# Kernel optimization log

Measured on AMD Instinct MI355X. Metric: run time of the kernel, lower is better.

Reference implementation:

```python
import jax, jax.numpy as jnp
import numpy as np

B, C, T = 8, 256, 4096
IC = C // 2  # inter_channels
BN_EPS = 1e-5


def setup_inputs() -> dict:
    key = jax.random.key(0)
    ks = jax.random.split(key, 12)
    s_in = 1.0 / np.sqrt(C)
    s_ic = 1.0 / np.sqrt(IC)
    return {
        "x": jax.random.normal(ks[0], (B, C, T), dtype=jnp.float32),
        "theta_w": jax.random.uniform(ks[1], (IC, C), jnp.float32, -s_in, s_in),
        "theta_b": jax.random.uniform(ks[2], (IC,), jnp.float32, -s_in, s_in),
        "phi_w": jax.random.uniform(ks[3], (IC, C), jnp.float32, -s_in, s_in),
        "phi_b": jax.random.uniform(ks[4], (IC,), jnp.float32, -s_in, s_in),
        "g_w": jax.random.uniform(ks[5], (IC, C), jnp.float32, -s_in, s_in),
        "g_b": jax.random.uniform(ks[6], (IC,), jnp.float32, -s_in, s_in),
        "w_w": jax.random.uniform(ks[7], (C, IC), jnp.float32, -s_ic, s_ic),
        "w_b": jax.random.uniform(ks[8], (C,), jnp.float32, -s_ic, s_ic),
        "bn_gamma": jax.random.normal(ks[9], (C,), dtype=jnp.float32),
        "bn_beta": jax.random.normal(ks[10], (C,), dtype=jnp.float32),
    }


def _conv1x1(w, b, inp):
    # Conv1d kernel_size=1 == per-position channel matmul
    return jnp.einsum('oc,bct->bot', w, inp) + b[None, :, None]


def _maxpool2(z):
    b, c, t = z.shape
    return z.reshape(b, c, t // 2, 2).max(axis=-1)


def reference(x, theta_w, theta_b, phi_w, phi_b, g_w, g_b, w_w, w_b, bn_gamma, bn_beta):
    theta_x = _conv1x1(theta_w, theta_b, x)              # (B, IC, T)
    phi_x = _maxpool2(_conv1x1(phi_w, phi_b, x))         # (B, IC, T/2)
    g_x = _maxpool2(_conv1x1(g_w, g_b, x))               # (B, IC, T/2)

    # f = theta^T @ phi ; softmax-free, divided by N = T/2
    f = jnp.einsum('bct,bcs->bts', theta_x, phi_x)       # (B, T, T/2)
    f_div_C = f / f.shape[-1]
    y = jnp.einsum('bts,bcs->bct', f_div_C, g_x)         # (B, IC, T)

    w_y = _conv1x1(w_w, w_b, y)                          # (B, C, T)
    # BatchNorm1d (training-mode batch statistics over batch+time)
    mean = w_y.mean(axis=(0, 2), keepdims=True)
    var = w_y.var(axis=(0, 2), keepdims=True)
    w_y = (w_y - mean) * jax.lax.rsqrt(var + BN_EPS)
    w_y = w_y * bn_gamma[None, :, None] + bn_beta[None, :, None]
    return w_y + x
```

## Files before the change

kernel.cpp:

```cpp
#include <hip/hip_runtime.h>
#include <hip/hip_bf16.h>

typedef __attribute__((ext_vector_type(8))) short short8;
typedef __attribute__((ext_vector_type(4))) short short4v;
typedef __attribute__((ext_vector_type(4))) float floatx4;
typedef unsigned int u32;

#define BB 8
#define CC 256
#define ICH 128
#define TT 4096
#define SS 2048
static constexpr float BN_EPS = 1e-5f;
static constexpr float INV_S  = 1.0f / 2048.0f;
static constexpr float INV_BT = 1.0f / 32768.0f;

typedef const __attribute__((address_space(1))) u32* gas_ptr;
typedef __attribute__((address_space(3))) u32* las_ptr;
__device__ __forceinline__ void gl_lds16(const void* g, void* l) {
    __builtin_amdgcn_global_load_lds((gas_ptr)g, (las_ptr)l, 16, 0, 0);
}

__global__ __launch_bounds__(256) void k0x_transpose(
    const float* __restrict__ x, __hip_bfloat16* __restrict__ xt)
{
    __shared__ float Tl[64][65];
    const int b = blockIdx.z, cb = blockIdx.y * 64, tb = blockIdx.x * 64;
    const int tid = threadIdx.x;
    #pragma unroll
    for (int it = 0; it < 4; ++it) {
        int idx = tid + 256 * it;
        int row = idx >> 4, c4 = idx & 15;
        float4 v = *(const float4*)(x + ((size_t)b * CC + cb + row) * TT + tb + c4 * 4);
        Tl[row][c4 * 4 + 0] = v.x; Tl[row][c4 * 4 + 1] = v.y;
        Tl[row][c4 * 4 + 2] = v.z; Tl[row][c4 * 4 + 3] = v.w;
    }
    __syncthreads();
    #pragma unroll
    for (int it = 0; it < 2; ++it) {
        int idx = tid + 256 * it;
        int trow = idx >> 3, ch = idx & 7;
        alignas(16) __hip_bfloat16 tmp[8];
        #pragma unroll
        for (int e = 0; e < 8; ++e) tmp[e] = __float2bfloat16(Tl[ch * 8 + e][trow]);
        *(short8*)(xt + ((size_t)b * TT + tb + trow) * CC + cb + ch * 8) = *(const short8*)tmp;
    }
}

__global__ __launch_bounds__(256) void k0w_conv(
    const float* __restrict__ phi_w, const float* __restrict__ g_w,
    __hip_bfloat16* __restrict__ Wf)
{
    int idx = blockIdx.x * 256 + threadIdx.x;
    const float* src = (idx < 8192) ? (phi_w + (size_t)idx * 4)
                                    : (g_w + (size_t)(idx - 8192) * 4);
    float4 v = *(const float4*)src;
    alignas(8) __hip_bfloat16 t[4];
    t[0] = __float2bfloat16(v.x); t[1] = __float2bfloat16(v.y);
    t[2] = __float2bfloat16(v.z); t[3] = __float2bfloat16(v.w);
    *(short4v*)(Wf + (size_t)idx * 4) = *(const short4v*)t;
}

__global__ __launch_bounds__(256) void k1_mfma(
    const __hip_bfloat16* __restrict__ Wf, const float* __restrict__ phi_b,
    const float* __restrict__ g_b, const __hip_bfloat16* __restrict__ xt,
    __hip_bfloat16* __restrict__ phi_g)
{
    __shared__ short lds[128 * 132];
    short* As = lds;
    short* Bs = lds + 128 * 64;

    const int b  = blockIdx.z;
    const int m0 = blockIdx.y * 128;
    const int tb = blockIdx.x * 128;
    const int s0 = blockIdx.x * 64;
    const int tid = threadIdx.x;
    const int w = tid >> 6, l = tid & 63;
    const int quad = l >> 4, lm = l & 15;
    const int wm = (w & 1) * 64, wn = (w >> 1) * 64;
    const int rs = l >> 3, cs = (l & 7) * 8;

    const __hip_bfloat16* Ap = Wf + (size_t)m0 * CC;
    const __hip_bfloat16* Bp = xt + ((size_t)b * TT + tb) * CC;

    floatx4 acc[4][4];
    #pragma unroll
    for (int i = 0; i < 4; ++i)
        #pragma unroll
        for (int j = 0; j < 4; ++j) acc[i][j] = (floatx4)0.f;

    for (int kc = 0; kc < 4; ++kc) {
        const int k0 = kc * 64;
        const int rbase = w * 32;
        #pragma unroll
        for (int t = 0; t < 4; ++t) {
            gl_lds16(Ap + (size_t)(rbase + t * 8 + rs) * CC + k0 + cs, &As[(rbase + t * 8) * 64]);
            gl_lds16(Bp + (size_t)(rbase + t * 8 + rs) * CC + k0 + cs, &Bs[(rbase + t * 8) * 64]);
        }
        __syncthreads();
        #pragma unroll
        for (int ks = 0; ks < 2; ++ks) {
            short8 a[4], bb[4];
            #pragma unroll
            for (int i = 0; i < 4; ++i)
                a[i] = *(const short8*)&As[(wm + i * 16 + lm) * 64 + ks * 32 + quad * 8];
            #pragma unroll
            for (int j = 0; j < 4; ++j)
                bb[j] = *(const short8*)&Bs[(wn + j * 16 + lm) * 64 + ks * 32 + quad * 8];
            #pragma unroll
            for (int i = 0; i < 4; ++i)
                #pragma unroll
                for (int j = 0; j < 4; ++j)
                    acc[i][j] = __builtin_amdgcn_mfma_f32_16x16x32_bf16(a[i], bb[j], acc[i][j], 0, 0, 0);
        }
        __syncthreads();
    }

    __hip_bfloat16* Out = (__hip_bfloat16*)lds;
    #pragma unroll
    for (int i = 0; i < 4; ++i)
        #pragma unroll
        for (int j = 0; j < 4; ++j)
            #pragma unroll
            for (int r = 0; r < 4; ++r)
                Out[(wm + i * 16 + quad * 4 + r) * 132 + wn + j * 16 + lm] =
                    __float2bfloat16(acc[i][j][r]);
    __syncthreads();
    #pragma unroll
    for (int it = 0; it < 4; ++it) {
        int idx = tid + 256 * it;
        int orow = idx >> 3, grp = idx & 7;
        int o = m0 + orow;
        float bias = (o < ICH) ? phi_b[o] : g_b[o - ICH];
        short8 v0 = *(const short8*)&Out[orow * 132 + grp * 16];
        short8 v1 = *(const short8*)&Out[orow * 132 + grp * 16 + 8];
        const __hip_bfloat16* p0 = (const __hip_bfloat16*)&v0;
        const __hip_bfloat16* p1 = (const __hip_bfloat16*)&v1;
        alignas(16) __hip_bfloat16 o8[8];
        #pragma unroll
        for (int e = 0; e < 4; ++e)
            o8[e] = __float2bfloat16(
                fmaxf(__bfloat162float(p0[2 * e]), __bfloat162float(p0[2 * e + 1])) + bias);
        #pragma unroll
        for (int e = 0; e < 4; ++e)
            o8[4 + e] = __float2bfloat16(
                fmaxf(__bfloat162float(p1[2 * e]), __bfloat162float(p1[2 * e + 1])) + bias);
        *(short8*)(phi_g + ((size_t)b * CC + o) * SS + s0 + grp * 8) = *(const short8*)o8;
    }
}

__global__ __launch_bounds__(256) void k2_mfma(
    const __hip_bfloat16* __restrict__ phi_g, float* __restrict__ Mpart)
{
    __shared__ short lds[2 * 128 * 64];
    short* As = lds;
    short* Bs = lds + 128 * 64;
    const int sc = blockIdx.x, b = blockIdx.y;
    const int tid = threadIdx.x;
    const int w = tid >> 6, l = tid & 63;
    const int quad = l >> 4, lm = l & 15;
    const int wm = (w & 1) * 64, wn = (w >> 1) * 64;
    const int rs = l >> 3, cs = (l & 7) * 8;

    const __hip_bfloat16* Ap = phi_g + (size_t)b * CC * SS + sc * 128;
    const __hip_bfloat16* Bp = Ap + (size_t)ICH * SS;

    floatx4 acc[4][4];
    #pragma unroll
    for (int i = 0; i < 4; ++i)
        #pragma unroll
        for (int j = 0; j < 4; ++j) acc[i][j] = (floatx4)0.f;

    for (int kc = 0; kc < 2; ++kc) {
        const int k0 = kc * 64;
        const int rbase = w * 32;
        #pragma unroll
        for (int t = 0; t < 4; ++t) {
            gl_lds16(Ap + (size_t)(rbase + t * 8 + rs) * SS + k0 + cs, &As[(rbase + t * 8) * 64]);
            gl_lds16(Bp + (size_t)(rbase + t * 8 + rs) * SS + k0 + cs, &Bs[(rbase + t * 8) * 64]);
        }
        __syncthreads();
        #pragma unroll
        for (int ks = 0; ks < 2; ++ks) {
            short8 a[4], bb[4];
            #pragma unroll
            for (int i = 0; i < 4; ++i)
                a[i] = *(const short8*)&As[(wm + i * 16 + lm) * 64 + ks * 32 + quad * 8];
            #pragma unroll
            for (int j = 0; j < 4; ++j)
                bb[j] = *(const short8*)&Bs[(wn + j * 16 + lm) * 64 + ks * 32 + quad * 8];
            #pragma unroll
            for (int i = 0; i < 4; ++i)
                #pragma unroll
                for (int j = 0; j < 4; ++j)
                    acc[i][j] = __builtin_amdgcn_mfma_f32_16x16x32_bf16(a[i], bb[j], acc[i][j], 0, 0, 0);
        }
        __syncthreads();
    }

    float* dst = Mpart + ((size_t)(b * 16 + sc)) * ICH * ICH;
    #pragma unroll
    for (int i = 0; i < 4; ++i)
        #pragma unroll
        for (int j = 0; j < 4; ++j)
            #pragma unroll
            for (int r = 0; r < 4; ++r)
                dst[(size_t)(wm + i * 16 + quad * 4 + r) * ICH + wn + j * 16 + lm] = acc[i][j][r];
}

__global__ __launch_bounds__(256) void k2b_reduce(
    const float* __restrict__ Mpart, float* __restrict__ Msum)
{
    const int b = blockIdx.y;
    const size_t f4 = (size_t)blockIdx.x * 256 + threadIdx.x;
    const float* src = Mpart + (size_t)b * 16 * 16384 + f4 * 4;
    float4 s = {0.f, 0.f, 0.f, 0.f};
    #pragma unroll
    for (int sc = 0; sc < 16; ++sc) {
        float4 v = *(const float4*)(src + (size_t)sc * 16384);
        s.x += v.x; s.y += v.y; s.z += v.z; s.w += v.w;
    }
    *(float4*)(Msum + (size_t)b * 16384 + f4 * 4) = s;
}

__global__ __launch_bounds__(256) void k3a_kb(
    const float* __restrict__ w_w, const float* __restrict__ Msum,
    float* __restrict__ Kb)
{
    __shared__ float Al[64][65];
    __shared__ float Bl[64][65];
    const int b = blockIdx.z;
    const int cob = blockIdx.y * 64;
    const int cpb = blockIdx.x * 64;
    const int tid = threadIdx.x;
    const int tx = tid & 15, ty = tid >> 4;

    float acc[4][4] = {};
    for (int kc2 = 0; kc2 < 2; ++kc2) {
        #pragma unroll
        for (int r = 0; r < 4; ++r) {
            int idx = tid + 256 * r;
            int row = idx >> 4, c4 = idx & 15;
            float4 v = *(const float4*)(w_w + (size_t)(cob + row) * ICH + kc2 * 64 + c4 * 4);
            Al[c4 * 4 + 0][row] = v.x; Al[c4 * 4 + 1][row] = v.y;
            Al[c4 * 4 + 2][row] = v.z; Al[c4 * 4 + 3][row] = v.w;
            float4 m = *(const float4*)(Msum + ((size_t)b * ICH + cpb + row) * ICH + kc2 * 64 + c4 * 4);
            Bl[c4 * 4 + 0][row] = m.x; Bl[c4 * 4 + 1][row] = m.y;
            Bl[c4 * 4 + 2][row] = m.z; Bl[c4 * 4 + 3][row] = m.w;
        }
        __syncthreads();
        for (int k = 0; k < 64; ++k) {
            float av[4], bv[4];
            #pragma unroll
            for (int i = 0; i < 4; ++i) av[i] = Al[k][ty + 16 * i];
            #pragma unroll
            for (int j = 0; j < 4; ++j) bv[j] = Bl[k][tx + 16 * j];
            #pragma unroll
            for (int i = 0; i < 4; ++i)
                #pragma unroll
                for (int j = 0; j < 4; ++j) acc[i][j] += av[i] * bv[j];
        }
        __syncthreads();
    }
    #pragma unroll
    for (int i = 0; i < 4; ++i)
        #pragma unroll
        for (int j = 0; j < 4; ++j)
            Kb[((size_t)b * CC + cob + ty + 16 * i) * ICH + cpb + tx + 16 * j] = acc[i][j] * INV_S;
}

__global__ __launch_bounds__(256) void k3b_p(
    const float* __restrict__ Kb, const float* __restrict__ theta_w,
    __hip_bfloat16* __restrict__ P)
{
    __shared__ float Al[64][65];
    __shared__ float Bl[64][128];
    const int b = blockIdx.z;
    const int cob = blockIdx.y * 64;
    const int cib = blockIdx.x * 128;
    const int tid = threadIdx.x;
    const int tx = tid & 15, ty = tid >> 4;

    float acc[4][8] = {};
    for (int kc2 = 0; kc2 < 2; ++kc2) {
        #pragma unroll
        for (int r = 0; r < 4; ++r) {
            int idx = tid + 256 * r;
            int row = idx >> 4, c4 = idx & 15;
            float4 v = *(const float4*)(Kb + ((size_t)b * CC + cob + row) * ICH + kc2 * 64 + c4 * 4);
            Al[c4 * 4 + 0][row] = v.x; Al[c4 * 4 + 1][row] = v.y;
            Al[c4 * 4 + 2][row] = v.z; Al[c4 * 4 + 3][row] = v.w;
        }
        #pragma unroll
        for (int r = 0; r < 8; ++r) {
            int idx = tid + 256 * r;
            int row = idx >> 5, c4 = idx & 31;
            *(float4*)(&Bl[row][c4 * 4]) =
                *(const float4*)(theta_w + (size_t)(kc2 * 64 + row) * CC + cib + c4 * 4);
        }
        __syncthreads();
        for (int k = 0; k < 64; ++k) {
            float av[4], bv[8];
            #pragma unroll
            for (int i = 0; i < 4; ++i) av[i] = Al[k][ty + 16 * i];
            #pragma unroll
            for (int j = 0; j < 8; ++j) bv[j] = Bl[k][tx + 16 * j];
            #pragma unroll
            for (int i = 0; i < 4; ++i)
                #pragma unroll
                for (int j = 0; j < 8; ++j) acc[i][j] += av[i] * bv[j];
        }
        __syncthreads();
    }
    #pragma unroll
    for (int i = 0; i < 4; ++i)
        #pragma unroll
        for (int j = 0; j < 8; ++j)
            P[((size_t)b * CC + cob + ty + 16 * i) * CC + cib + tx + 16 * j] =
                __float2bfloat16(acc[i][j]);
}

__global__ __launch_bounds__(256) void k3c_q(
    const float* __restrict__ Kb, const float* __restrict__ theta_b,
    const float* __restrict__ w_b, float* __restrict__ q)
{
    __shared__ float tbs[ICH];
    const int b = blockIdx.x, co = threadIdx.x;
    if (co < ICH) tbs[co] = theta_b[co];
    __syncthreads();
    const float* kr = Kb + ((size_t)b * CC + co) * ICH;
    float s = w_b[co];
    for (int c = 0; c < ICH; ++c) s += kr[c] * tbs[c];
    q[b * CC + co] = s;
}

__global__ __launch_bounds__(256) void k4_mfma(
    const __hip_bfloat16* __restrict__ P, const __hip_bfloat16* __restrict__ xt,
    const float* __restrict__ q, __hip_bfloat16* __restrict__ wy,
    float* __restrict__ pbuf)
{
    __shared__ short lds[128 * 132];
    __shared__ float pst1[4 * 64], pst2[4 * 64];
    short* As = lds;
    short* Bs = lds + 128 * 64;

    const int b  = blockIdx.z;
    const int m0 = blockIdx.y * 128;
    const int t0 = blockIdx.x * 128;
    const int tid = threadIdx.x;
    const int w = tid >> 6, l = tid & 63;
    const int quad = l >> 4, lm = l & 15;
    const int wm = (w & 1) * 64, wn = (w >> 1) * 64;
    const int rs = l >> 3, cs = (l & 7) * 8;

    const __hip_bfloat16* Ap = P + ((size_t)b * CC + m0) * CC;
    const __hip_bfloat16* Bp = xt + ((size_t)b * TT + t0) * CC;

    floatx4 acc[4][4];
    #pragma unroll
    for (int i = 0; i < 4; ++i)
        #pragma unroll
        for (int j = 0; j < 4; ++j) acc[i][j] = (floatx4)0.f;

    for (int kc = 0; kc < 4; ++kc) {
        const int k0 = kc * 64;
        const int rbase = w * 32;
        #pragma unroll
        for (int t = 0; t < 4; ++t) {
            gl_lds16(Ap + (size_t)(rbase + t * 8 + rs) * CC + k0 + cs, &As[(rbase + t * 8) * 64]);
            gl_lds16(Bp + (size_t)(rbase + t * 8 + rs) * CC + k0 + cs, &Bs[(rbase + t * 8) * 64]);
        }
        __syncthreads();
        #pragma unroll
        for (int ks = 0; ks < 2; ++ks) {
            short8 a[4], bb[4];
            #pragma unroll
            for (int i = 0; i < 4; ++i)
                a[i] = *(const short8*)&As[(wm + i * 16 + lm) * 64 + ks * 32 + quad * 8];
            #pragma unroll
            for (int j = 0; j < 4; ++j)
                bb[j] = *(const short8*)&Bs[(wn + j * 16 + lm) * 64 + ks * 32 + quad * 8];
            #pragma unroll
            for (int i = 0; i < 4; ++i)
                #pragma unroll
                for (int j = 0; j < 4; ++j)
                    acc[i][j] = __builtin_amdgcn_mfma_f32_16x16x32_bf16(a[i], bb[j], acc[i][j], 0, 0, 0);
        }
        __syncthreads();
    }

    #pragma unroll
    for (int i = 0; i < 4; ++i) {
        #pragma unroll
        for (int r = 0; r < 4; ++r) {
            int m = wm + i * 16 + quad * 4 + r;
            float bias = q[b * CC + m0 + m];
            float s1 = 0.f, s2 = 0.f;
            #pragma unroll
            for (int j = 0; j < 4; ++j) {
                float v = acc[i][j][r] + bias;
                s1 += v; s2 += v * v;
            }
            #pragma unroll
            for (int off = 1; off < 16; off <<= 1) {
                s1 += __shfl_xor(s1, off);
                s2 += __shfl_xor(s2, off);
            }
            if (lm == 0) {
                pst1[w * 64 + i * 16 + quad * 4 + r] = s1;
                pst2[w * 64 + i * 16 + quad * 4 + r] = s2;
            }
        }
    }

    __hip_bfloat16* Out = (__hip_bfloat16*)lds;
    #pragma unroll
    for (int i = 0; i < 4; ++i) {
        #pragma unroll
        for (int r = 0; r < 4; ++r) {
            int m = wm + i * 16 + quad * 4 + r;
            float bias = q[b * CC + m0 + m];
            #pragma unroll
            for (int j = 0; j < 4; ++j)
                Out[m * 132 + wn + j * 16 + lm] = __float2bfloat16(acc[i][j][r] + bias);
        }
    }
    __syncthreads();

    if (tid < 128) {
        int half = tid >> 6, k = tid & 63;
        float s1 = pst1[half * 64 + k] + pst1[(2 + half) * 64 + k];
        float s2 = pst2[half * 64 + k] + pst2[(2 + half) * 64 + k];
        size_t col = (size_t)b * 32 + blockIdx.x;
        pbuf[(size_t)(m0 + tid) * 256 + col] = s1;
        pbuf[65536 + (size_t)(m0 + tid) * 256 + col] = s2;
    }

    #pragma unroll
    for (int it = 0; it < 8; ++it) {
        int idx = tid + 256 * it;
        int row = idx >> 4, cg = idx & 15;
        *(short8*)(wy + ((size_t)b * CC + m0 + row) * TT + t0 + cg * 8) =
            *(const short8*)&Out[row * 132 + cg * 8];
    }
}

__global__ __launch_bounds__(256) void k5_bn(
    const float* __restrict__ pbuf, const float* __restrict__ gamma,
    const float* __restrict__ beta, float* __restrict__ coef)
{
    const int c = blockIdx.x, tid = threadIdx.x;
    float v1 = pbuf[(size_t)c * 256 + tid];
    float v2 = pbuf[65536 + (size_t)c * 256 + tid];
    #pragma unroll
    for (int off = 1; off < 64; off <<= 1) {
        v1 += __shfl_xor(v1, off);
        v2 += __shfl_xor(v2, off);
    }
    __shared__ float r1[4], r2[4];
    if ((tid & 63) == 0) { r1[tid >> 6] = v1; r2[tid >> 6] = v2; }
    __syncthreads();
    if (tid == 0) {
        float t1 = r1[0] + r1[1] + r1[2] + r1[3];
        float t2 = r2[0] + r2[1] + r2[2] + r2[3];
        float mean = t1 * INV_BT;
        float var  = t2 * INV_BT - mean * mean;
        float A = gamma[c] * rsqrtf(var + BN_EPS);
        coef[c] = A;
        coef[CC + c] = beta[c] - mean * A;
    }
}

__global__ __launch_bounds__(256) void k6_out(
    const __hip_bfloat16* __restrict__ wy, const __hip_bfloat16* __restrict__ xt,
    const float* __restrict__ coef, float* __restrict__ out)
{
    __shared__ float Fs[64][68];
    const int b = blockIdx.z, cb = blockIdx.y * 64, tb = blockIdx.x * 64;
    const int tid = threadIdx.x;

    {
        const int t = tid >> 2, cseg = (tid & 3) * 16;
        const __hip_bfloat16* src = xt + ((size_t)b * TT + tb + t) * CC + cb + cseg;
        short8 v0 = *(const short8*)src;
        short8 v1 = *(const short8*)(src + 8);
        const __hip_bfloat16* p0 = (const __hip_bfloat16*)&v0;
        const __hip_bfloat16* p1 = (const __hip_bfloat16*)&v1;
        #pragma unroll
        for (int e = 0; e < 8; ++e) Fs[t][cseg + e] = __bfloat162float(p0[e]);
        #pragma unroll
        for (int e = 0; e < 8; ++e) Fs[t][cseg + 8 + e] = __bfloat162float(p1[e]);
    }
    __syncthreads();

    const int c = tid >> 2, seg = (tid & 3) * 16;
    const float A = coef[cb + c], Bc = coef[CC + cb + c];
    const __hip_bfloat16* wsrc = wy + ((size_t)b * CC + cb + c) * TT + tb + seg;
    short8 w0 = *(const short8*)wsrc;
    short8 w1 = *(const short8*)(wsrc + 8);
    const __hip_bfloat16* q0 = (const __hip_bfloat16*)&w0;
    const __hip_bfloat16* q1 = (const __hip_bfloat16*)&w1;
    float* dst = out + ((size_t)b * CC + cb + c) * TT + tb + seg;
    #pragma unroll
    for (int e = 0; e < 8; ++e)
        dst[e] = __bfloat162float(q0[e]) * A + Bc + Fs[seg + e][c];
    #pragma unroll
    for (int e = 0; e < 8; ++e)
        dst[8 + e] = __bfloat162float(q1[e]) * A + Bc + Fs[seg + 8 + e][c];
}

extern "C" void kernel_launch(void* const* d_in, const int* in_sizes, int n_in,
                              void* d_out, int out_size, void* d_ws, size_t ws_size,
                              hipStream_t stream)
{
    const float* x        = (const float*)d_in[0];
    const float* theta_w  = (const float*)d_in[1];
    const float* theta_b  = (const float*)d_in[2];
    const float* phi_w    = (const float*)d_in[3];
    const float* phi_b    = (const float*)d_in[4];
    const float* g_w      = (const float*)d_in[5];
    const float* g_b      = (const float*)d_in[6];
    const float* w_w      = (const float*)d_in[7];
    const float* w_b      = (const float*)d_in[8];
    const float* bn_gamma = (const float*)d_in[9];
    const float* bn_beta  = (const float*)d_in[10];
    float* out = (float*)d_out;

    char* p = (char*)d_ws;
    __hip_bfloat16* xt    = (__hip_bfloat16*)p; p += (size_t)8388608 * 2;
    __hip_bfloat16* Wf    = (__hip_bfloat16*)p; p += (size_t)65536 * 2;
    __hip_bfloat16* phi_g = (__hip_bfloat16*)p; p += (size_t)4194304 * 2;
    __hip_bfloat16* P     = (__hip_bfloat16*)p; p += (size_t)524288 * 2;
    float* Mpart = (float*)p; p += (size_t)2097152 * 4;
    float* Msum  = (float*)p; p += (size_t)131072 * 4;
    float* Kb    = (float*)p; p += (size_t)262144 * 4;
    float* q     = (float*)p; p += (size_t)2048 * 4;
    __hip_bfloat16* wy = (__hip_bfloat16*)p; p += (size_t)8388608 * 2;
    float* pbuf  = (float*)p; p += (size_t)131072 * 4;
    float* coef  = (float*)p;

    k0x_transpose<<<dim3(64, 4, 8), 256, 0, stream>>>(x, xt);
    k0w_conv<<<dim3(64), 256, 0, stream>>>(phi_w, g_w, Wf);
    k1_mfma<<<dim3(32, 2, 8), 256, 0, stream>>>(Wf, phi_b, g_b, xt, phi_g);
    k2_mfma<<<dim3(16, 8), 256, 0, stream>>>(phi_g, Mpart);
    k2b_reduce<<<dim3(16, 8), 256, 0, stream>>>(Mpart, Msum);
    k3a_kb<<<dim3(2, 4, 8), 256, 0, stream>>>(w_w, Msum, Kb);
    k3b_p<<<dim3(2, 4, 8), 256, 0, stream>>>(Kb, theta_w, P);
    k3c_q<<<dim3(8), 256, 0, stream>>>(Kb, theta_b, w_b, q);
    k4_mfma<<<dim3(32, 2, 8), 256, 0, stream>>>(P, xt, q, wy, pbuf);
    k5_bn<<<dim3(256), 256, 0, stream>>>(pbuf, bn_gamma, bn_beta, coef);
    k6_out<<<dim3(64, 4, 8), 256, 0, stream>>>(wy, xt, coef, out);
}
```

Before: 181.8 us.

## Fold small kernels into neighbors and shrink k2 split-K partials

Weight conversion is merged into the transpose kernel as an extra z-slice, and the q computation is merged into k3b_p. k2 now splits S into 4 chunks of 512 instead of 16 chunks of 128, so the separate reduce kernel goes away and k3a sums the 4 partials while loading. This removes three launches and most of the partial-sum traffic. In exchange k2 runs only 32 blocks with longer loops, which leaves much of the GPU idle during that stage.

```diff
diff --git a/kernel.cpp b/kernel.cpp
--- a/kernel.cpp
+++ b/kernel.cpp
@@ -22,8 +22,23 @@
 }
 
 __global__ __launch_bounds__(256) void k0x_transpose(
-    const float* __restrict__ x, __hip_bfloat16* __restrict__ xt)
-{
+    const float* __restrict__ x, __hip_bfloat16* __restrict__ xt,
+    const float* __restrict__ phi_w, const float* __restrict__ g_w,
+    __hip_bfloat16* __restrict__ Wf)
+{
+    if (blockIdx.z == 8) {
+        if (blockIdx.y != 0) return;
+        int idx = blockIdx.x * 256 + threadIdx.x;
+        const float* src = (idx < 8192) ? (phi_w + (size_t)idx * 4)
+                                        : (g_w + (size_t)(idx - 8192) * 4);
+        float4 v = *(const float4*)src;
+        alignas(8) __hip_bfloat16 t[4];
+        t[0] = __float2bfloat16(v.x); t[1] = __float2bfloat16(v.y);
+        t[2] = __float2bfloat16(v.z); t[3] = __float2bfloat16(v.w);
+        *(short4v*)(Wf + (size_t)idx * 4) = *(const short4v*)t;
+        return;
+    }
+
     __shared__ float Tl[64][65];
     const int b = blockIdx.z, cb = blockIdx.y * 64, tb = blockIdx.x * 64;
     const int tid = threadIdx.x;
@@ -45,20 +60,6 @@
         for (int e = 0; e < 8; ++e) tmp[e] = __float2bfloat16(Tl[ch * 8 + e][trow]);
         *(short8*)(xt + ((size_t)b * TT + tb + trow) * CC + cb + ch * 8) = *(const short8*)tmp;
     }
-}
-
-__global__ __launch_bounds__(256) void k0w_conv(
-    const float* __restrict__ phi_w, const float* __restrict__ g_w,
-    __hip_bfloat16* __restrict__ Wf)
-{
-    int idx = blockIdx.x * 256 + threadIdx.x;
-    const float* src = (idx < 8192) ? (phi_w + (size_t)idx * 4)
-                                    : (g_w + (size_t)(idx - 8192) * 4);
-    float4 v = *(const float4*)src;
-    alignas(8) __hip_bfloat16 t[4];
-    t[0] = __float2bfloat16(v.x); t[1] = __float2bfloat16(v.y);
-    t[2] = __float2bfloat16(v.z); t[3] = __float2bfloat16(v.w);
-    *(short4v*)(Wf + (size_t)idx * 4) = *(const short4v*)t;
 }
 
 __global__ __launch_bounds__(256) void k1_mfma(
@@ -162,7 +163,7 @@
     const int wm = (w & 1) * 64, wn = (w >> 1) * 64;
     const int rs = l >> 3, cs = (l & 7) * 8;
 
-    const __hip_bfloat16* Ap = phi_g + (size_t)b * CC * SS + sc * 128;
+    const __hip_bfloat16* Ap = phi_g + (size_t)b * CC * SS + sc * 512;
     const __hip_bfloat16* Bp = Ap + (size_t)ICH * SS;
 
     floatx4 acc[4][4];
@@ -171,7 +172,7 @@
         #pragma unroll
         for (int j = 0; j < 4; ++j) acc[i][j] = (floatx4)0.f;
 
-    for (int kc = 0; kc < 2; ++kc) {
+    for (int kc = 0; kc < 8; ++kc) {
         const int k0 = kc * 64;
         const int rbase = w * 32;
         #pragma unroll
@@ -198,7 +199,7 @@
         __syncthreads();
     }
 
-    float* dst = Mpart + ((size_t)(b * 16 + sc)) * ICH * ICH;
+    float* dst = Mpart + ((size_t)(b * 4 + sc)) * ICH * ICH;
     #pragma unroll
     for (int i = 0; i < 4; ++i)
         #pragma unroll
@@ -208,23 +209,8 @@
                 dst[(size_t)(wm + i * 16 + quad * 4 + r) * ICH + wn + j * 16 + lm] = acc[i][j][r];
 }
 
-__global__ __launch_bounds__(256) void k2b_reduce(
-    const float* __restrict__ Mpart, float* __restrict__ Msum)
-{
-    const int b = blockIdx.y;
-    const size_t f4 = (size_t)blockIdx.x * 256 + threadIdx.x;
-    const float* src = Mpart + (size_t)b * 16 * 16384 + f4 * 4;
-    float4 s = {0.f, 0.f, 0.f, 0.f};
-    #pragma unroll
-    for (int sc = 0; sc < 16; ++sc) {
-        float4 v = *(const float4*)(src + (size_t)sc * 16384);
-        s.x += v.x; s.y += v.y; s.z += v.z; s.w += v.w;
-    }
-    *(float4*)(Msum + (size_t)b * 16384 + f4 * 4) = s;
-}
-
 __global__ __launch_bounds__(256) void k3a_kb(
-    const float* __restrict__ w_w, const float* __restrict__ Msum,
+    const float* __restrict__ w_w, const float* __restrict__ Mpart,
     float* __restrict__ Kb)
 {
     __shared__ float Al[64][65];
@@ -244,9 +230,14 @@
             float4 v = *(const float4*)(w_w + (size_t)(cob + row) * ICH + kc2 * 64 + c4 * 4);
             Al[c4 * 4 + 0][row] = v.x; Al[c4 * 4 + 1][row] = v.y;
             Al[c4 * 4 + 2][row] = v.z; Al[c4 * 4 + 3][row] = v.w;
-            float4 m = *(const float4*)(Msum + ((size_t)b * ICH + cpb + row) * ICH + kc2 * 64 + c4 * 4);
-            Bl[c4 * 4 + 0][row] = m.x; Bl[c4 * 4 + 1][row] = m.y;
-            Bl[c4 * 4 + 2][row] = m.z; Bl[c4 * 4 + 3][row] = m.w;
+            float4 s = {0.f, 0.f, 0.f, 0.f};
+            #pragma unroll
+            for (int sc = 0; sc < 4; ++sc) {
+                float4 m = *(const float4*)(Mpart + (((size_t)b * 4 + sc) * ICH + cpb + row) * ICH + kc2 * 64 + c4 * 4);
+                s.x += m.x; s.y += m.y; s.z += m.z; s.w += m.w;
+            }
+            Bl[c4 * 4 + 0][row] = s.x; Bl[c4 * 4 + 1][row] = s.y;
+            Bl[c4 * 4 + 2][row] = s.z; Bl[c4 * 4 + 3][row] = s.w;
         }
         __syncthreads();
         for (int k = 0; k < 64; ++k) {
@@ -271,7 +262,8 @@
 
 __global__ __launch_bounds__(256) void k3b_p(
     const float* __restrict__ Kb, const float* __restrict__ theta_w,
-    __hip_bfloat16* __restrict__ P)
+    const float* __restrict__ theta_b, const float* __restrict__ w_b,
+    __hip_bfloat16* __restrict__ P, float* __restrict__ q)
 {
     __shared__ float Al[64][65];
     __shared__ float Bl[64][128];
@@ -318,20 +310,14 @@
         for (int j = 0; j < 8; ++j)
             P[((size_t)b * CC + cob + ty + 16 * i) * CC + cib + tx + 16 * j] =
                 __float2bfloat16(acc[i][j]);
-}
-
-__global__ __launch_bounds__(256) void k3c_q(
-    const float* __restrict__ Kb, const float* __restrict__ theta_b,
-    const float* __restrict__ w_b, float* __restrict__ q)
-{
-    __shared__ float tbs[ICH];
-    const int b = blockIdx.x, co = threadIdx.x;
-    if (co < ICH) tbs[co] = theta_b[co];
-    __syncthreads();
-    const float* kr = Kb + ((size_t)b * CC + co) * ICH;
-    float s = w_b[co];
-    for (int c = 0; c < ICH; ++c) s += kr[c] * tbs[c];
-    q[b * CC + co] = s;
+
+    if (blockIdx.x == 0 && tid < 64) {
+        const float* kr = Kb + ((size_t)b * CC + cob + tid) * ICH;
+        float s = w_b[cob + tid];
+        #pragma unroll 8
+        for (int c = 0; c < ICH; ++c) s += kr[c] * theta_b[c];
+        q[b * CC + cob + tid] = s;
+    }
 }
 
 __global__ __launch_bounds__(256) void k4_mfma(
@@ -531,22 +517,18 @@
     __hip_bfloat16* Wf    = (__hip_bfloat16*)p; p += (size_t)65536 * 2;
     __hip_bfloat16* phi_g = (__hip_bfloat16*)p; p += (size_t)4194304 * 2;
     __hip_bfloat16* P     = (__hip_bfloat16*)p; p += (size_t)524288 * 2;
-    float* Mpart = (float*)p; p += (size_t)2097152 * 4;
-    float* Msum  = (float*)p; p += (size_t)131072 * 4;
+    float* Mpart = (float*)p; p += (size_t)524288 * 4;
     float* Kb    = (float*)p; p += (size_t)262144 * 4;
     float* q     = (float*)p; p += (size_t)2048 * 4;
     __hip_bfloat16* wy = (__hip_bfloat16*)p; p += (size_t)8388608 * 2;
     float* pbuf  = (float*)p; p += (size_t)131072 * 4;
     float* coef  = (float*)p;
 
-    k0x_transpose<<<dim3(64, 4, 8), 256, 0, stream>>>(x, xt);
-    k0w_conv<<<dim3(64), 256, 0, stream>>>(phi_w, g_w, Wf);
+    k0x_transpose<<<dim3(64, 4, 9), 256, 0, stream>>>(x, xt, phi_w, g_w, Wf);
     k1_mfma<<<dim3(32, 2, 8), 256, 0, stream>>>(Wf, phi_b, g_b, xt, phi_g);
-    k2_mfma<<<dim3(16, 8), 256, 0, stream>>>(phi_g, Mpart);
-    k2b_reduce<<<dim3(16, 8), 256, 0, stream>>>(Mpart, Msum);
-    k3a_kb<<<dim3(2, 4, 8), 256, 0, stream>>>(w_w, Msum, Kb);
-    k3b_p<<<dim3(2, 4, 8), 256, 0, stream>>>(Kb, theta_w, P);
-    k3c_q<<<dim3(8), 256, 0, stream>>>(Kb, theta_b, w_b, q);
+    k2_mfma<<<dim3(4, 8), 256, 0, stream>>>(phi_g, Mpart);
+    k3a_kb<<<dim3(2, 4, 8), 256, 0, stream>>>(w_w, Mpart, Kb);
+    k3b_p<<<dim3(2, 4, 8), 256, 0, stream>>>(Kb, theta_w, theta_b, w_b, P, q);
     k4_mfma<<<dim3(32, 2, 8), 256, 0, stream>>>(P, xt, q, wy, pbuf);
     k5_bn<<<dim3(256), 256, 0, stream>>>(pbuf, bn_gamma, bn_beta, coef);
     k6_out<<<dim3(64, 4, 8), 256, 0, stream>>>(wy, xt, coef, out);
```

Result: no change. 180.3 us (-0.8%).
